# Performance work log

Measured on AMD Instinct MI355X. Metric: run time of the kernel, lower is better.

Reference implementation:

```python
import jax, jax.numpy as jnp
import numpy as np

SEQ = 4096
EMBED = 1024


def setup_inputs() -> dict:
    key = jax.random.key(0)
    k1, k2 = jax.random.split(key)
    x = jax.random.normal(k1, (SEQ, EMBED), dtype=jnp.float32)
    # torch Linear(embed, 3*embed): store transposed weight so y = x @ W + b
    W = jax.random.normal(k2, (EMBED, 3 * EMBED), dtype=jnp.float32) * (1.0 / np.sqrt(EMBED))
    b = jnp.zeros((3 * EMBED,), dtype=jnp.float32)
    return {"x": x, "W": W, "b": b}


def reference(x, W, b):
    # QKV projection: [S, 3E] -> chunk along features
    qkv = x @ W + b
    q, k, v = jnp.split(qkv, 3, axis=1)  # each [S, E]
    d = q.shape[-1]
    scale = jnp.sqrt(jnp.asarray(d, dtype=x.dtype))
    logits = (q @ k.T) / scale  # [S, S]
    S = q.shape[0]
    causal = jnp.triu(jnp.ones((S, S), dtype=bool), k=1)
    logits = jnp.where(causal, -jnp.inf, logits)
    w = jax.nn.softmax(logits, axis=1)
    return w @ v  # [S, E]
```

## Files before the change

kernel.cpp:

```cpp
#include <hip/hip_runtime.h>

typedef short s16x8 __attribute__((ext_vector_type(8)));
typedef unsigned short u16;
typedef u16 u16x8 __attribute__((ext_vector_type(8)));
typedef float f32x4 __attribute__((ext_vector_type(4)));

#define SEQ 4096
#define EMBED 1024
#define NQKV 3072

static __device__ __forceinline__ u16 f2bf(float f) {
  unsigned int u = __float_as_uint(f);
  u += 0x7fffu + ((u >> 16) & 1u);
  return (u16)(u >> 16);
}
static __device__ __forceinline__ float bf2f(u16 b) {
  return __uint_as_float(((unsigned int)b) << 16);
}

static __device__ __forceinline__ f32x4 mfma16(s16x8 a, s16x8 b, f32x4 c) {
  return __builtin_amdgcn_mfma_f32_16x16x32_bf16(a, b, c, 0, 0, 0);
}

static __device__ __forceinline__ void gl2lds(const u16* g, u16* l) {
  __builtin_amdgcn_global_load_lds(
      (const __attribute__((address_space(1))) unsigned int*)g,
      (__attribute__((address_space(3))) unsigned int*)l, 16, 0, 0);
}

#define WAITVM(n) asm volatile("s_waitcnt vmcnt(" #n ")" ::: "memory")
#define LGKM0 asm volatile("s_waitcnt lgkmcnt(0)" ::: "memory")
#define BAR() asm volatile("s_waitcnt lgkmcnt(0)\n\ts_barrier" ::: "memory")

__global__ __launch_bounds__(256) void conv_x(const float* __restrict__ x,
                                              u16* __restrict__ xbf) {
  const size_t base = ((size_t)blockIdx.x * 256 + threadIdx.x) * 16;
  u16 tmp[16];
#pragma unroll
  for (int p = 0; p < 4; ++p) {
    float4 v = *reinterpret_cast<const float4*>(&x[base + p * 4]);
    tmp[p * 4 + 0] = f2bf(v.x); tmp[p * 4 + 1] = f2bf(v.y);
    tmp[p * 4 + 2] = f2bf(v.z); tmp[p * 4 + 3] = f2bf(v.w);
  }
  *reinterpret_cast<u16x8*>(&xbf[base]) = *reinterpret_cast<u16x8*>(&tmp[0]);
  *reinterpret_cast<u16x8*>(&xbf[base + 8]) = *reinterpret_cast<u16x8*>(&tmp[8]);
}

__global__ __launch_bounds__(256) void conv_wT(const float* __restrict__ W,
                                               u16* __restrict__ wT) {
  __shared__ u16 t[64][72];
  const int n0 = blockIdx.x * 64;
  const int k0 = blockIdx.y * 64;
  const int tid = threadIdx.x;
  const int rr = tid >> 3, c8 = (tid & 7) * 8;
#pragma unroll
  for (int p = 0; p < 2; ++p) {
    int r = p * 32 + rr;
    float4 a = *reinterpret_cast<const float4*>(&W[(size_t)(k0 + r) * NQKV + n0 + c8]);
    float4 b = *reinterpret_cast<const float4*>(&W[(size_t)(k0 + r) * NQKV + n0 + c8 + 4]);
    t[r][c8 + 0] = f2bf(a.x); t[r][c8 + 1] = f2bf(a.y);
    t[r][c8 + 2] = f2bf(a.z); t[r][c8 + 3] = f2bf(a.w);
    t[r][c8 + 4] = f2bf(b.x); t[r][c8 + 5] = f2bf(b.y);
    t[r][c8 + 6] = f2bf(b.z); t[r][c8 + 7] = f2bf(b.w);
  }
  __syncthreads();
#pragma unroll
  for (int p = 0; p < 2; ++p) {
    int c = p * 32 + rr;
    u16x8 v;
#pragma unroll
    for (int j = 0; j < 8; ++j) v[j] = t[c8 + j][c];
    *reinterpret_cast<u16x8*>(&wT[(size_t)(n0 + c) * EMBED + k0 + c8]) = v;
  }
}

#define GSTAGE32(dst, srcbase, stride)                                        \
  {                                                                           \
    _Pragma("unroll") for (int p_ = 0; p_ < 2; ++p_) {                        \
      gl2lds((srcbase) + (size_t)(p_ * 64 + w * 16 + (l >> 2)) * (stride) +   \
                 (l & 3) * 8,                                                 \
             (dst) + p_ * 2048 + w * 512);                                    \
    }                                                                         \
  }

#define MFMA_STEP(Acur, Bcur)                                                 \
  {                                                                           \
    s16x8 af[4], bfr[4];                                                      \
    _Pragma("unroll") for (int mb = 0; mb < 4; ++mb)                          \
        af[mb] = *reinterpret_cast<const s16x8*>(&(Acur)[(wr + mb * 16 + lr) * 32 + lg * 8]); \
    _Pragma("unroll") for (int nb = 0; nb < 4; ++nb)                          \
        bfr[nb] = *reinterpret_cast<const s16x8*>(&(Bcur)[(wc + nb * 16 + lr) * 32 + lg * 8]); \
    _Pragma("unroll") for (int mb = 0; mb < 4; ++mb)                          \
        _Pragma("unroll") for (int nb = 0; nb < 4; ++nb)                      \
            acc[mb][nb] = mfma16(af[mb], bfr[nb], acc[mb][nb]);               \
  }

#define KLOOP(n, SRC_A, SA_STRIDE, SRC_B, SB_STRIDE)                          \
  GSTAGE32(As[0], SRC_A(0), SA_STRIDE);                                       \
  GSTAGE32(Bs[0], SRC_B(0), SB_STRIDE);                                       \
  GSTAGE32(As[1], SRC_A(1), SA_STRIDE);                                       \
  GSTAGE32(Bs[1], SRC_B(1), SB_STRIDE);                                       \
  for (int t = 0; t < (n); ++t) {                                             \
    const int cur = t % 3;                                                    \
    if (t + 2 < (n)) {                                                        \
      LGKM0;                                                                  \
      const int nx = (t + 2) % 3;                                             \
      GSTAGE32(As[nx], SRC_A(t + 2), SA_STRIDE);                              \
      GSTAGE32(Bs[nx], SRC_B(t + 2), SB_STRIDE);                              \
      WAITVM(8);                                                              \
    } else if (t + 1 < (n)) {                                                 \
      WAITVM(4);                                                              \
    } else {                                                                  \
      WAITVM(0);                                                              \
    }                                                                         \
    BAR();                                                                    \
    MFMA_STEP(As[cur], Bs[cur]);                                              \
    BAR();                                                                    \
  }

__global__ __launch_bounds__(256) void qkv_gemm(const u16* __restrict__ xbf,
                                                const u16* __restrict__ wT,
                                                const float* __restrict__ bias,
                                                u16* __restrict__ qkv) {
  __shared__ u16 As[3][4096];
  __shared__ u16 Bs[3][4096];
  const int b = blockIdx.x;
  const int bs = (b & 7) * 96 + (b >> 3);
  const int bm = bs / 24, bn = bs % 24;
  const int m0 = bm * 128, n0 = bn * 128;
  const int tid = threadIdx.x;
  const int w = tid >> 6, l = tid & 63;
  const int wr = (w >> 1) * 64, wc = (w & 1) * 64;
  const int lg = l >> 4, lr = l & 15;

  f32x4 acc[4][4];
#pragma unroll
  for (int i = 0; i < 4; ++i)
#pragma unroll
    for (int j = 0; j < 4; ++j) acc[i][j] = (f32x4){0.f, 0.f, 0.f, 0.f};

  const u16* xa = xbf + (size_t)m0 * EMBED;
  const u16* wb = wT + (size_t)n0 * EMBED;
#define QA_SRC(t) (xa + (t) * 32)
#define QB_SRC(t) (wb + (t) * 32)
  KLOOP(32, QA_SRC, EMBED, QB_SRC, EMBED);
#undef QA_SRC
#undef QB_SRC

#pragma unroll
  for (int mb = 0; mb < 4; ++mb)
#pragma unroll
    for (int nb = 0; nb < 4; ++nb) {
      const int col = n0 + wc + nb * 16 + lr;
      const float bv = bias[col];
#pragma unroll
      for (int e = 0; e < 4; ++e) {
        const int row = m0 + wr + mb * 16 + lg * 4 + e;
        qkv[(size_t)row * NQKV + col] = f2bf(acc[mb][nb][e] + bv);
      }
    }
}

__global__ __launch_bounds__(256) void v_transpose(const u16* __restrict__ qkv,
                                                   u16* __restrict__ vT) {
  __shared__ u16 t[64][72];
  const int s0 = blockIdx.x * 64;
  const int c0 = blockIdx.y * 64;
  const int tid = threadIdx.x;
  const int rr = tid >> 3, c8 = (tid & 7) * 8;
#pragma unroll
  for (int p = 0; p < 2; ++p) {
    int r = p * 32 + rr;
    *reinterpret_cast<u16x8*>(&t[r][c8]) =
        *reinterpret_cast<const u16x8*>(&qkv[(size_t)(s0 + r) * NQKV + 2 * EMBED + c0 + c8]);
  }
  __syncthreads();
#pragma unroll
  for (int p = 0; p < 2; ++p) {
    int c = p * 32 + rr;
    u16x8 v;
#pragma unroll
    for (int j = 0; j < 8; ++j) v[j] = t[c8 + j][c];
    *reinterpret_cast<u16x8*>(&vT[(size_t)(c0 + c) * SEQ + s0 + c8]) = v;
  }
}

__global__ __launch_bounds__(256) void s_gemm(const u16* __restrict__ qkv,
                                              u16* __restrict__ Sp) {
  __shared__ u16 As[3][4096];
  __shared__ u16 Bs[3][4096];
  const int b = blockIdx.x;
  const int bs = (b & 7) * 66 + (b >> 3);
  int mt = 0, cum = 0;
  while (cum + mt + 1 <= bs) { cum += mt + 1; ++mt; }
  const int nt = bs - cum;
  const int m0 = mt * 128, n0 = nt * 128;
  const int tid = threadIdx.x;
  const int w = tid >> 6, l = tid & 63;
  const int wr = (w >> 1) * 64, wc = (w & 1) * 64;
  const int lg = l >> 4, lr = l & 15;

  f32x4 acc[4][4];
#pragma unroll
  for (int i = 0; i < 4; ++i)
#pragma unroll
    for (int j = 0; j < 4; ++j) acc[i][j] = (f32x4){0.f, 0.f, 0.f, 0.f};

  const u16* qa = qkv + (size_t)m0 * NQKV;
  const u16* kb = qkv + (size_t)n0 * NQKV + EMBED;
#define SA_SRC(t) (qa + (t) * 32)
#define SB_SRC(t) (kb + (t) * 32)
  KLOOP(32, SA_SRC, NQKV, SB_SRC, NQKV);
#undef SA_SRC
#undef SB_SRC

  u16* base = Sp + (size_t)bs * 16384;
#pragma unroll
  for (int mb = 0; mb < 4; ++mb)
#pragma unroll
    for (int nb = 0; nb < 4; ++nb) {
      const int cn = wc + nb * 16 + lr;
#pragma unroll
      for (int e = 0; e < 4; ++e) {
        const int rm = wr + mb * 16 + lg * 4 + e;
        base[rm * 128 + cn] = f2bf(acc[mb][nb][e] * 0.03125f);
      }
    }
}

__global__ __launch_bounds__(256) void softmax_rows(u16* __restrict__ Sp) {
  __shared__ float red[8];
  const int bid = blockIdx.x;
  const int tid = threadIdx.x;
  const int w = tid >> 6, l = tid & 63;
  const float NEG = -3.0e38f;

  for (int half = 0; half < 2; ++half) {
    const int r = half ? (4095 - bid) : bid;
    const int mt = r >> 7, rr = r & 127;
    const int Lp = (mt + 1) << 7;
    const size_t tri = (size_t)mt * (mt + 1) / 2;

    float v[16];
    float mx = NEG;
#pragma unroll
    for (int s = 0; s < 2; ++s) {
      const int j = tid * 8 + s * 2048;
      if (j < Lp) {
        const u16* p = Sp + (tri + (j >> 7)) * 16384 + rr * 128 + (j & 127);
        u16x8 xv = *reinterpret_cast<const u16x8*>(p);
#pragma unroll
        for (int e = 0; e < 8; ++e) {
          float f = (j + e <= r) ? bf2f(xv[e]) : NEG;
          v[s * 8 + e] = f;
          mx = fmaxf(mx, f);
        }
      } else {
#pragma unroll
        for (int e = 0; e < 8; ++e) v[s * 8 + e] = NEG;
      }
    }
#pragma unroll
    for (int off = 32; off >= 1; off >>= 1) mx = fmaxf(mx, __shfl_xor(mx, off, 64));
    if (l == 0) red[w] = mx;
    __syncthreads();
    mx = fmaxf(fmaxf(red[0], red[1]), fmaxf(red[2], red[3]));

    float sum = 0.f;
#pragma unroll
    for (int i = 0; i < 16; ++i) {
      float e = __expf(v[i] - mx);
      v[i] = e;
      sum += e;
    }
#pragma unroll
    for (int off = 32; off >= 1; off >>= 1) sum += __shfl_xor(sum, off, 64);
    if (l == 0) red[4 + w] = sum;
    __syncthreads();
    sum = red[4] + red[5] + red[6] + red[7];
    const float inv = 1.f / sum;

#pragma unroll
    for (int s = 0; s < 2; ++s) {
      const int j = tid * 8 + s * 2048;
      if (j < Lp) {
        u16x8 pk;
#pragma unroll
        for (int e = 0; e < 8; ++e) pk[e] = f2bf(v[s * 8 + e] * inv);
        *reinterpret_cast<u16x8*>(Sp + (tri + (j >> 7)) * 16384 + rr * 128 + (j & 127)) = pk;
      }
    }
    __syncthreads();
  }
}

__global__ __launch_bounds__(256) void pv_gemm(const u16* __restrict__ Sp,
                                               const u16* __restrict__ vT,
                                               float* __restrict__ out) {
  __shared__ u16 As[3][4096];
  __shared__ u16 Bs[3][4096];
  const int nt = blockIdx.y;
  int sx = blockIdx.x;
  int mt = 0, cum = 0, ls = 0;
  for (;;) {
    const int ns = (mt + 4) >> 2;
    if (sx < cum + ns) { ls = sx - cum; break; }
    cum += ns; ++mt;
  }
  const int m0 = mt * 128, n0 = nt * 128;
  const int k0 = ls * 512;
  const int kext = (mt + 1) * 128;
  const int kend = (k0 + 512 < kext) ? (k0 + 512) : kext;
  const int ksteps = (kend - k0) >> 5;
  const size_t tri = (size_t)mt * (mt + 1) / 2;

  const int tid = threadIdx.x;
  const int w = tid >> 6, l = tid & 63;
  const int wr = (w >> 1) * 64, wc = (w & 1) * 64;
  const int lg = l >> 4, lr = l & 15;

  f32x4 acc[4][4];
#pragma unroll
  for (int i = 0; i < 4; ++i)
#pragma unroll
    for (int j = 0; j < 4; ++j) acc[i][j] = (f32x4){0.f, 0.f, 0.f, 0.f};

#define PA_SRC(t) (Sp + (tri + ((k0 + (t)*32) >> 7)) * 16384 + ((k0 + (t)*32) & 127))
#define PB_SRC(t) (vT + (size_t)n0 * SEQ + k0 + (t)*32)
  KLOOP(ksteps, PA_SRC, 128, PB_SRC, SEQ);
#undef PA_SRC
#undef PB_SRC

#pragma unroll
  for (int mb = 0; mb < 4; ++mb)
#pragma unroll
    for (int nb = 0; nb < 4; ++nb) {
      const int col = n0 + wc + nb * 16 + lr;
#pragma unroll
      for (int e = 0; e < 4; ++e) {
        const int row = m0 + wr + mb * 16 + lg * 4 + e;
        unsafeAtomicAdd(&out[(size_t)row * EMBED + col], acc[mb][nb][e]);
      }
    }
}

__global__ __launch_bounds__(512) void attn_fb(const u16* __restrict__ qkv,
                                               const u16* __restrict__ vT,
                                               float* __restrict__ out) {
  __shared__ u16 q_lds[16][1032];
  __shared__ u16 kv_lds[8][3][2048];
  __shared__ u16 p_lds[16][136];
  __shared__ float redmax[8][16];
  __shared__ float redsum[8][16];
  const int bid = blockIdx.x;
  const int tid = threadIdx.x;
  const int w = tid >> 6, l = tid & 63;
  const int lg = l >> 4, lr = l & 15;

  const int sr = l >> 4;
  const int scb = (l & 15) * 16;
  const int scolA = ((scb ^ (sr << 4)) >> 1);
  const int scolB = ((scb ^ ((4 + sr) << 4)) >> 1);
  int boff[4];
#pragma unroll
  for (int kk = 0; kk < 4; ++kk)
    boff[kk] = lr * 256 + ((kk * 64 + lg * 16) ^ ((lr & 7) << 4));

  u16* kvb[3] = {&kv_lds[w][0][0], &kv_lds[w][1][0], &kv_lds[w][2][0]};

#define STAGE_K(dc, bufp)                                                     \
  {                                                                           \
    LGKM0;                                                                    \
    const u16* g0 = qkv + (size_t)(kb + w * 16 + sr) * NQKV + EMBED + (dc) * 128; \
    gl2lds(g0 + scolA, (bufp));                                               \
    gl2lds(g0 + 4 * NQKV + scolB, (bufp) + 512);                              \
    gl2lds(g0 + 8 * NQKV + scolA, (bufp) + 1024);                             \
    gl2lds(g0 + 12 * NQKV + scolB, (bufp) + 1536);                            \
  }
#define STAGE_V(j, bufp)                                                      \
  {                                                                           \
    LGKM0;                                                                    \
    const u16* g0 = vT + (size_t)((j) * 128 + w * 16 + sr) * SEQ + kb;        \
    gl2lds(g0 + scolA, (bufp));                                               \
    gl2lds(g0 + 4 * SEQ + scolB, (bufp) + 512);                               \
    gl2lds(g0 + 8 * SEQ + scolA, (bufp) + 1024);                              \
    gl2lds(g0 + 12 * SEQ + scolB, (bufp) + 1536);                             \
  }

  const int qb = bid * 16;
  __syncthreads();
#pragma unroll
  for (int p = 0; p < 4; ++p) {
    int idx = p * 512 + tid;
    int r = idx >> 7, c = (idx & 127) * 8;
    *reinterpret_cast<u16x8*>(&q_lds[r][c]) =
        *reinterpret_cast<const u16x8*>(&qkv[(size_t)(qb + r) * NQKV + c]);
  }
  __syncthreads();
  s16x8 qf[32];
#pragma unroll
  for (int kk = 0; kk < 32; ++kk)
    qf[kk] = *reinterpret_cast<const s16x8*>(&q_lds[lr][kk * 32 + lg * 8]);

  f32x4 o_acc[8];
#pragma unroll
  for (int j = 0; j < 8; ++j) o_acc[j] = (f32x4){0.f, 0.f, 0.f, 0.f};
  float m_st[4], l_st[4];
#pragma unroll
  for (int e = 0; e < 4; ++e) { m_st[e] = -__builtin_inff(); l_st[e] = 0.f; }

  const int n_it = (qb >> 7) + 1;
  for (int it = 0; it < n_it; ++it) {
    const int kb = it << 7;
    const int kcol = kb + w * 16 + lr;

    f32x4 s = (f32x4){0.f, 0.f, 0.f, 0.f};
    STAGE_K(0, kvb[0]);
    STAGE_K(1, kvb[1]);
#pragma unroll
    for (int dc = 0; dc < 8; ++dc) {
      if (dc < 6) {
        STAGE_K(dc + 2, kvb[(dc + 2) % 3]);
      } else if (dc == 6) {
        STAGE_V(0, kvb[2]);
      } else {
        STAGE_V(1, kvb[0]);
      }
      WAITVM(8);
      u16* cur = kvb[dc % 3];
#pragma unroll
      for (int kk = 0; kk < 4; ++kk) {
        s16x8 bfr = *reinterpret_cast<const s16x8*>((const char*)cur + boff[kk]);
        s = mfma16(qf[dc * 4 + kk], bfr, s);
      }
    }

    float sv[4], mx[4];
#pragma unroll
    for (int e = 0; e < 4; ++e) {
      float v = s[e] * 0.03125f;
      sv[e] = (kcol > qb + lg * 4 + e) ? -__builtin_inff() : v;
      mx[e] = sv[e];
    }
#pragma unroll
    for (int off = 1; off < 16; off <<= 1)
#pragma unroll
      for (int e = 0; e < 4; ++e) mx[e] = fmaxf(mx[e], __shfl_xor(mx[e], off, 64));
    if (lr == 0) {
#pragma unroll
      for (int e = 0; e < 4; ++e) redmax[w][lg * 4 + e] = mx[e];
    }
    BAR();

    float m_new[4], sc[4], pv[4], rs[4];
#pragma unroll
    for (int e = 0; e < 4; ++e) {
      float m = m_st[e];
#pragma unroll
      for (int ww = 0; ww < 8; ++ww) m = fmaxf(m, redmax[ww][lg * 4 + e]);
      m_new[e] = m;
      sc[e] = __expf(m_st[e] - m);
      pv[e] = __expf(sv[e] - m);
      rs[e] = pv[e];
    }
#pragma unroll
    for (int off = 1; off < 16; off <<= 1)
#pragma unroll
      for (int e = 0; e < 4; ++e) rs[e] += __shfl_xor(rs[e], off, 64);
    if (lr == 0) {
#pragma unroll
      for (int e = 0; e < 4; ++e) redsum[w][lg * 4 + e] = rs[e];
    }
#pragma unroll
    for (int e = 0; e < 4; ++e) p_lds[lg * 4 + e][w * 16 + lr] = f2bf(pv[e]);
    BAR();

#pragma unroll
    for (int e = 0; e < 4; ++e) {
      float a2 = l_st[e] * sc[e];
#pragma unroll
      for (int ww = 0; ww < 8; ++ww) a2 += redsum[ww][lg * 4 + e];
      l_st[e] = a2;
      m_st[e] = m_new[e];
    }
#pragma unroll
    for (int j = 0; j < 8; ++j)
#pragma unroll
      for (int e = 0; e < 4; ++e) o_acc[j][e] *= sc[e];

    s16x8 pa[4];
#pragma unroll
    for (int kk = 0; kk < 4; ++kk)
      pa[kk] = *reinterpret_cast<const s16x8*>(&p_lds[lr][kk * 32 + lg * 8]);

#pragma unroll
    for (int j = 0; j < 8; ++j) {
      if (j < 6) {
        STAGE_V(j + 2, kvb[(j + 4) % 3]);
        WAITVM(8);
      } else if (j == 6) {
        WAITVM(4);
      } else {
        WAITVM(0);
      }
      u16* cur = kvb[(j + 2) % 3];
#pragma unroll
      for (int kk = 0; kk < 4; ++kk) {
        s16x8 bfr = *reinterpret_cast<const s16x8*>((const char*)cur + boff[kk]);
        o_acc[j] = mfma16(pa[kk], bfr, o_acc[j]);
      }
    }
  }

#pragma unroll
  for (int j = 0; j < 8; ++j) {
    const int col = j * 128 + w * 16 + lr;
#pragma unroll
    for (int e = 0; e < 4; ++e)
      out[(size_t)(qb + lg * 4 + e) * EMBED + col] = o_acc[j][e] / l_st[e];
  }
#undef STAGE_K
#undef STAGE_V
}

extern "C" void kernel_launch(void* const* d_in, const int* in_sizes, int n_in,
                              void* d_out, int out_size, void* d_ws, size_t ws_size,
                              hipStream_t stream) {
  (void)in_sizes; (void)n_in; (void)out_size;
  const float* x = (const float*)d_in[0];
  const float* W = (const float*)d_in[1];
  const float* bias = (const float*)d_in[2];
  float* out = (float*)d_out;

  u16* qkv = (u16*)d_ws;
  u16* vT = qkv + (size_t)SEQ * NQKV;
  u16* xbf = vT;
  u16* wT = (u16*)d_out;
  u16* Sp = (u16*)((char*)d_ws + (32u << 20));

  const size_t need = (32u << 20) + (size_t)528 * 16384 * 2;

  conv_x<<<(SEQ * EMBED) / (256 * 16), 256, 0, stream>>>(x, xbf);
  conv_wT<<<dim3(NQKV / 64, EMBED / 64), 256, 0, stream>>>(W, wT);
  qkv_gemm<<<(SEQ / 128) * (NQKV / 128), 256, 0, stream>>>(xbf, wT, bias, qkv);
  v_transpose<<<dim3(SEQ / 64, EMBED / 64), 256, 0, stream>>>(qkv, vT);

  if (ws_size >= need) {
    s_gemm<<<528, 256, 0, stream>>>(qkv, Sp);
    softmax_rows<<<2048, 256, 0, stream>>>(Sp);
    hipMemsetAsync(d_out, 0, (size_t)SEQ * EMBED * sizeof(float), stream);
    pv_gemm<<<dim3(144, 8), 256, 0, stream>>>(Sp, vT, out);
  } else {
    attn_fb<<<SEQ / 16, 512, 0, stream>>>(qkv, vT, out);
  }
}
```

Before: 180.4 us.

## Use 256x256 tiles with 8 waves and interleaved prefetch/MFMA phases in GEMMs

All three GEMMs (QKV, scores, PV) move from 128x128 tiles with 4 waves to 256x256 tiles with 8 waves. They now share a core loop that splits each k-step into four phases, each overlapping one global-to-LDS stage load with MFMA work, with barriers and s_setprio between phases. The larger tiles cut global/LDS traffic per flop and the phasing aims to hide load latency. The cost is far fewer blocks (192, 136 and 160), which can leave CUs idle on a large GPU and worsens load imbalance across causal triangle tiles.

Result: faster. 161.4 us (-10.5%).

```diff
diff --git a/kernel.cpp b/kernel.cpp
--- a/kernel.cpp
+++ b/kernel.cpp
@@ -30,7 +30,7 @@
 
 #define WAITVM(n) asm volatile("s_waitcnt vmcnt(" #n ")" ::: "memory")
 #define LGKM0 asm volatile("s_waitcnt lgkmcnt(0)" ::: "memory")
-#define BAR() asm volatile("s_waitcnt lgkmcnt(0)\n\ts_barrier" ::: "memory")
+#define BARRIER() __builtin_amdgcn_s_barrier()
 
 __global__ __launch_bounds__(256) void conv_x(const float* __restrict__ x,
                                               u16* __restrict__ xbf) {
@@ -74,89 +74,94 @@
   }
 }
 
-#define GSTAGE32(dst, srcbase, stride)                                        \
+
+#define G256_PHASE(p, stgsrc, stgdst_off)                                     \
   {                                                                           \
-    _Pragma("unroll") for (int p_ = 0; p_ < 2; ++p_) {                        \
-      gl2lds((srcbase) + (size_t)(p_ * 64 + w * 16 + (l >> 2)) * (stride) +   \
-                 (l & 3) * 8,                                                 \
-             (dst) + p_ * 2048 + w * 512);                                    \
+    s16x8 a0_ = *reinterpret_cast<const s16x8*>(                              \
+        &lds_[aoff_ + (wm * 128 + (2 * (p)) * 16 + lr) * 32 + lg * 8]);       \
+    s16x8 a1_ = *reinterpret_cast<const s16x8*>(                              \
+        &lds_[aoff_ + (wm * 128 + (2 * (p) + 1) * 16 + lr) * 32 + lg * 8]);   \
+    if (stg_) gl2lds((stgsrc), lds_ + (stgdst_off) + w * 512);                \
+    BARRIER();                                                                \
+    LGKM0;                                                                    \
+    __builtin_amdgcn_s_setprio(1);                                            \
+    _Pragma("unroll") for (int ni = 0; ni < 4; ++ni) {                        \
+      acc[2 * (p)][ni] = mfma16(a0_, bf_[ni], acc[2 * (p)][ni]);              \
+      acc[2 * (p) + 1][ni] = mfma16(a1_, bf_[ni], acc[2 * (p) + 1][ni]);      \
     }                                                                         \
-  }
-
-#define MFMA_STEP(Acur, Bcur)                                                 \
-  {                                                                           \
-    s16x8 af[4], bfr[4];                                                      \
-    _Pragma("unroll") for (int mb = 0; mb < 4; ++mb)                          \
-        af[mb] = *reinterpret_cast<const s16x8*>(&(Acur)[(wr + mb * 16 + lr) * 32 + lg * 8]); \
-    _Pragma("unroll") for (int nb = 0; nb < 4; ++nb)                          \
-        bfr[nb] = *reinterpret_cast<const s16x8*>(&(Bcur)[(wc + nb * 16 + lr) * 32 + lg * 8]); \
-    _Pragma("unroll") for (int mb = 0; mb < 4; ++mb)                          \
-        _Pragma("unroll") for (int nb = 0; nb < 4; ++nb)                      \
-            acc[mb][nb] = mfma16(af[mb], bfr[nb], acc[mb][nb]);               \
-  }
-
-#define KLOOP(n, SRC_A, SA_STRIDE, SRC_B, SB_STRIDE)                          \
-  GSTAGE32(As[0], SRC_A(0), SA_STRIDE);                                       \
-  GSTAGE32(Bs[0], SRC_B(0), SB_STRIDE);                                       \
-  GSTAGE32(As[1], SRC_A(1), SA_STRIDE);                                       \
-  GSTAGE32(Bs[1], SRC_B(1), SB_STRIDE);                                       \
-  for (int t = 0; t < (n); ++t) {                                             \
-    const int cur = t % 3;                                                    \
-    if (t + 2 < (n)) {                                                        \
-      LGKM0;                                                                  \
-      const int nx = (t + 2) % 3;                                             \
-      GSTAGE32(As[nx], SRC_A(t + 2), SA_STRIDE);                              \
-      GSTAGE32(Bs[nx], SRC_B(t + 2), SB_STRIDE);                              \
-      WAITVM(8);                                                              \
-    } else if (t + 1 < (n)) {                                                 \
-      WAITVM(4);                                                              \
-    } else {                                                                  \
-      WAITVM(0);                                                              \
-    }                                                                         \
-    BAR();                                                                    \
-    MFMA_STEP(As[cur], Bs[cur]);                                              \
-    BAR();                                                                    \
-  }
-
-__global__ __launch_bounds__(256) void qkv_gemm(const u16* __restrict__ xbf,
+    __builtin_amdgcn_s_setprio(0);                                            \
+  }
+
+#define G256_CORE(NSTEPS, SRCA, SRCB)                                         \
+  f32x4 acc[8][4];                                                            \
+  _Pragma("unroll") for (int i_ = 0; i_ < 8; ++i_)                            \
+  _Pragma("unroll") for (int j_ = 0; j_ < 4; ++j_)                            \
+      acc[i_][j_] = (f32x4){0.f, 0.f, 0.f, 0.f};                              \
+  gl2lds(SRCA(0, 0), lds_ + w * 512);                                         \
+  gl2lds(SRCA(0, 1), lds_ + 4096 + w * 512);                                  \
+  gl2lds(SRCB(0, 0), lds_ + 24576 + w * 512);                                 \
+  gl2lds(SRCB(0, 1), lds_ + 24576 + 4096 + w * 512);                          \
+  gl2lds(SRCA(1, 0), lds_ + 8192 + w * 512);                                  \
+  gl2lds(SRCA(1, 1), lds_ + 8192 + 4096 + w * 512);                           \
+  gl2lds(SRCB(1, 0), lds_ + 24576 + 8192 + w * 512);                          \
+  gl2lds(SRCB(1, 1), lds_ + 24576 + 8192 + 4096 + w * 512);                   \
+  WAITVM(4);                                                                  \
+  BARRIER();                                                                  \
+  int cb_ = 0;                                                                \
+  for (int kt = 0; kt < (NSTEPS); ++kt) {                                     \
+    int nb_ = cb_ + 2; if (nb_ >= 3) nb_ -= 3;                                \
+    const int aoff_ = cb_ * 8192;                                             \
+    const int boff_ = 24576 + cb_ * 8192;                                     \
+    const int an_ = nb_ * 8192;                                               \
+    const int bn_ = 24576 + nb_ * 8192;                                       \
+    const bool stg_ = (kt + 2) < (NSTEPS);                                    \
+    s16x8 bf_[4];                                                             \
+    _Pragma("unroll") for (int ni = 0; ni < 4; ++ni)                          \
+        bf_[ni] = *reinterpret_cast<const s16x8*>(                            \
+            &lds_[boff_ + (wn * 64 + ni * 16 + lr) * 32 + lg * 8]);           \
+    G256_PHASE(0, SRCA(kt + 2, 0), an_)                                       \
+    BARRIER();                                                                \
+    G256_PHASE(1, SRCA(kt + 2, 1), an_ + 4096)                                \
+    BARRIER();                                                                \
+    G256_PHASE(2, SRCB(kt + 2, 0), bn_)                                       \
+    BARRIER();                                                                \
+    G256_PHASE(3, SRCB(kt + 2, 1), bn_ + 4096)                                \
+    if (stg_) { WAITVM(4); } else { WAITVM(0); }                              \
+    BARRIER();                                                                \
+    cb_ = (cb_ + 1 == 3) ? 0 : cb_ + 1;                                       \
+  }
+
+__global__ __launch_bounds__(512) void qkv_gemm(const u16* __restrict__ xbf,
                                                 const u16* __restrict__ wT,
                                                 const float* __restrict__ bias,
                                                 u16* __restrict__ qkv) {
-  __shared__ u16 As[3][4096];
-  __shared__ u16 Bs[3][4096];
+  __shared__ u16 lds_[49152];
   const int b = blockIdx.x;
-  const int bs = (b & 7) * 96 + (b >> 3);
-  const int bm = bs / 24, bn = bs % 24;
-  const int m0 = bm * 128, n0 = bn * 128;
+  const int bs = (b & 7) * 24 + (b >> 3);
+  const int m0 = (bs / 12) * 256, n0 = (bs % 12) * 256;
   const int tid = threadIdx.x;
   const int w = tid >> 6, l = tid & 63;
-  const int wr = (w >> 1) * 64, wc = (w & 1) * 64;
+  const int wm = w >> 2, wn = w & 3;
   const int lg = l >> 4, lr = l & 15;
 
-  f32x4 acc[4][4];
-#pragma unroll
-  for (int i = 0; i < 4; ++i)
-#pragma unroll
-    for (int j = 0; j < 4; ++j) acc[i][j] = (f32x4){0.f, 0.f, 0.f, 0.f};
-
-  const u16* xa = xbf + (size_t)m0 * EMBED;
-  const u16* wb = wT + (size_t)n0 * EMBED;
-#define QA_SRC(t) (xa + (t) * 32)
-#define QB_SRC(t) (wb + (t) * 32)
-  KLOOP(32, QA_SRC, EMBED, QB_SRC, EMBED);
-#undef QA_SRC
-#undef QB_SRC
-
-#pragma unroll
-  for (int mb = 0; mb < 4; ++mb)
-#pragma unroll
-    for (int nb = 0; nb < 4; ++nb) {
-      const int col = n0 + wc + nb * 16 + lr;
+  const u16* Ab = xbf + (size_t)m0 * EMBED;
+  const u16* Bb = wT + (size_t)n0 * EMBED;
+#define QSRCA(kt, i) (Ab + (size_t)(((i)*8 + w) * 16 + (l >> 2)) * EMBED + (kt)*32 + (l & 3) * 8)
+#define QSRCB(kt, i) (Bb + (size_t)(((i)*8 + w) * 16 + (l >> 2)) * EMBED + (kt)*32 + (l & 3) * 8)
+  G256_CORE(32, QSRCA, QSRCB)
+#undef QSRCA
+#undef QSRCB
+
+#pragma unroll
+  for (int mi = 0; mi < 8; ++mi)
+#pragma unroll
+    for (int ni = 0; ni < 4; ++ni) {
+      const int col = n0 + wn * 64 + ni * 16 + lr;
       const float bv = bias[col];
 #pragma unroll
       for (int e = 0; e < 4; ++e) {
-        const int row = m0 + wr + mb * 16 + lg * 4 + e;
-        qkv[(size_t)row * NQKV + col] = f2bf(acc[mb][nb][e] + bv);
+        const int row = m0 + wm * 128 + mi * 16 + lg * 4 + e;
+        qkv[(size_t)row * NQKV + col] = f2bf(acc[mi][ni][e] + bv);
       }
     }
 }
@@ -185,45 +190,38 @@
   }
 }
 
-__global__ __launch_bounds__(256) void s_gemm(const u16* __restrict__ qkv,
+__global__ __launch_bounds__(512) void s_gemm(const u16* __restrict__ qkv,
                                               u16* __restrict__ Sp) {
-  __shared__ u16 As[3][4096];
-  __shared__ u16 Bs[3][4096];
+  __shared__ u16 lds_[49152];
   const int b = blockIdx.x;
-  const int bs = (b & 7) * 66 + (b >> 3);
+  const int bs = (b & 7) * 17 + (b >> 3);
   int mt = 0, cum = 0;
   while (cum + mt + 1 <= bs) { cum += mt + 1; ++mt; }
   const int nt = bs - cum;
-  const int m0 = mt * 128, n0 = nt * 128;
+  const int m0 = mt * 256, n0 = nt * 256;
   const int tid = threadIdx.x;
   const int w = tid >> 6, l = tid & 63;
-  const int wr = (w >> 1) * 64, wc = (w & 1) * 64;
+  const int wm = w >> 2, wn = w & 3;
   const int lg = l >> 4, lr = l & 15;
 
-  f32x4 acc[4][4];
-#pragma unroll
-  for (int i = 0; i < 4; ++i)
-#pragma unroll
-    for (int j = 0; j < 4; ++j) acc[i][j] = (f32x4){0.f, 0.f, 0.f, 0.f};
-
-  const u16* qa = qkv + (size_t)m0 * NQKV;
-  const u16* kb = qkv + (size_t)n0 * NQKV + EMBED;
-#define SA_SRC(t) (qa + (t) * 32)
-#define SB_SRC(t) (kb + (t) * 32)
-  KLOOP(32, SA_SRC, NQKV, SB_SRC, NQKV);
-#undef SA_SRC
-#undef SB_SRC
-
-  u16* base = Sp + (size_t)bs * 16384;
-#pragma unroll
-  for (int mb = 0; mb < 4; ++mb)
-#pragma unroll
-    for (int nb = 0; nb < 4; ++nb) {
-      const int cn = wc + nb * 16 + lr;
+  const u16* Ab = qkv + (size_t)m0 * NQKV;
+  const u16* Bb = qkv + (size_t)n0 * NQKV + EMBED;
+#define SSRCA(kt, i) (Ab + (size_t)(((i)*8 + w) * 16 + (l >> 2)) * NQKV + (kt)*32 + (l & 3) * 8)
+#define SSRCB(kt, i) (Bb + (size_t)(((i)*8 + w) * 16 + (l >> 2)) * NQKV + (kt)*32 + (l & 3) * 8)
+  G256_CORE(32, SSRCA, SSRCB)
+#undef SSRCA
+#undef SSRCB
+
+  u16* base = Sp + (size_t)bs * 65536;
+#pragma unroll
+  for (int mi = 0; mi < 8; ++mi)
+#pragma unroll
+    for (int ni = 0; ni < 4; ++ni) {
+      const int cn = wn * 64 + ni * 16 + lr;
 #pragma unroll
       for (int e = 0; e < 4; ++e) {
-        const int rm = wr + mb * 16 + lg * 4 + e;
-        base[rm * 128 + cn] = f2bf(acc[mb][nb][e] * 0.03125f);
+        const int rm = wm * 128 + mi * 16 + lg * 4 + e;
+        base[rm * 256 + cn] = f2bf(acc[mi][ni][e] * 0.03125f);
       }
     }
 }
@@ -237,8 +235,8 @@
 
   for (int half = 0; half < 2; ++half) {
     const int r = half ? (4095 - bid) : bid;
-    const int mt = r >> 7, rr = r & 127;
-    const int Lp = (mt + 1) << 7;
+    const int mt = r >> 8, rr = r & 255;
+    const int Lp = (mt + 1) << 8;
     const size_t tri = (size_t)mt * (mt + 1) / 2;
 
     float v[16];
@@ -247,7 +245,7 @@
     for (int s = 0; s < 2; ++s) {
       const int j = tid * 8 + s * 2048;
       if (j < Lp) {
-        const u16* p = Sp + (tri + (j >> 7)) * 16384 + rr * 128 + (j & 127);
+        const u16* p = Sp + (tri + (j >> 8)) * 65536 + rr * 256 + (j & 255);
         u16x8 xv = *reinterpret_cast<const u16x8*>(p);
 #pragma unroll
         for (int e = 0; e < 8; ++e) {
@@ -287,59 +285,60 @@
         u16x8 pk;
 #pragma unroll
         for (int e = 0; e < 8; ++e) pk[e] = f2bf(v[s * 8 + e] * inv);
-        *reinterpret_cast<u16x8*>(Sp + (tri + (j >> 7)) * 16384 + rr * 128 + (j & 127)) = pk;
+        *reinterpret_cast<u16x8*>(Sp + (tri + (j >> 8)) * 65536 + rr * 256 + (j & 255)) = pk;
       }
     }
     __syncthreads();
   }
 }
 
-__global__ __launch_bounds__(256) void pv_gemm(const u16* __restrict__ Sp,
+__global__ __launch_bounds__(512) void pv_gemm(const u16* __restrict__ Sp,
                                                const u16* __restrict__ vT,
                                                float* __restrict__ out) {
-  __shared__ u16 As[3][4096];
-  __shared__ u16 Bs[3][4096];
-  const int nt = blockIdx.y;
-  int sx = blockIdx.x;
-  int mt = 0, cum = 0, ls = 0;
+  __shared__ u16 lds_[49152];
+  const int b = blockIdx.x;
+  const int bs = (b & 7) * 20 + (b >> 3);
+  int sx = bs, mt = 0, cum = 0;
   for (;;) {
-    const int ns = (mt + 4) >> 2;
-    if (sx < cum + ns) { ls = sx - cum; break; }
-    cum += ns; ++mt;
-  }
-  const int m0 = mt * 128, n0 = nt * 128;
-  const int k0 = ls * 512;
-  const int kext = (mt + 1) * 128;
-  const int kend = (k0 + 512 < kext) ? (k0 + 512) : kext;
+    const int cnt = ((mt + 4) >> 2) * 4;
+    if (sx < cum + cnt) break;
+    cum += cnt; ++mt;
+  }
+  const int rem = sx - cum;
+  const int ns = (mt + 4) >> 2;
+  const int nt = rem / ns, ls = rem % ns;
+  const int m0 = mt * 256, n0 = nt * 256;
+  const int k0 = ls * 1024;
+  const int kext = (mt + 1) << 8;
+  const int kend = (k0 + 1024 < kext) ? (k0 + 1024) : kext;
   const int ksteps = (kend - k0) >> 5;
   const size_t tri = (size_t)mt * (mt + 1) / 2;
 
   const int tid = threadIdx.x;
   const int w = tid >> 6, l = tid & 63;
-  const int wr = (w >> 1) * 64, wc = (w & 1) * 64;
+  const int wm = w >> 2, wn = w & 3;
   const int lg = l >> 4, lr = l & 15;
 
-  f32x4 acc[4][4];
-#pragma unroll
-  for (int i = 0; i < 4; ++i)
-#pragma unroll
-    for (int j = 0; j < 4; ++j) acc[i][j] = (f32x4){0.f, 0.f, 0.f, 0.f};
-
-#define PA_SRC(t) (Sp + (tri + ((k0 + (t)*32) >> 7)) * 16384 + ((k0 + (t)*32) & 127))
-#define PB_SRC(t) (vT + (size_t)n0 * SEQ + k0 + (t)*32)
-  KLOOP(ksteps, PA_SRC, 128, PB_SRC, SEQ);
-#undef PA_SRC
-#undef PB_SRC
-
-#pragma unroll
-  for (int mb = 0; mb < 4; ++mb)
-#pragma unroll
-    for (int nb = 0; nb < 4; ++nb) {
-      const int col = n0 + wc + nb * 16 + lr;
+#define PSRCA(kt, i)                                                          \
+  (Sp + (tri + ((unsigned)(k0 + (kt)*32) >> 8)) * 65536 +                     \
+   (size_t)(((i)*8 + w) * 16 + (l >> 2)) * 256 + ((k0 + (kt)*32) & 255) +     \
+   (l & 3) * 8)
+#define PSRCB(kt, i)                                                          \
+  (vT + (size_t)(n0 + ((i)*8 + w) * 16 + (l >> 2)) * SEQ + k0 + (kt)*32 +     \
+   (l & 3) * 8)
+  G256_CORE(ksteps, PSRCA, PSRCB)
+#undef PSRCA
+#undef PSRCB
+
+#pragma unroll
+  for (int mi = 0; mi < 8; ++mi)
+#pragma unroll
+    for (int ni = 0; ni < 4; ++ni) {
+      const int col = n0 + wn * 64 + ni * 16 + lr;
 #pragma unroll
       for (int e = 0; e < 4; ++e) {
-        const int row = m0 + wr + mb * 16 + lg * 4 + e;
-        unsafeAtomicAdd(&out[(size_t)row * EMBED + col], acc[mb][nb][e]);
+        const int row = m0 + wm * 128 + mi * 16 + lg * 4 + e;
+        unsafeAtomicAdd(&out[(size_t)row * EMBED + col], acc[mi][ni][e]);
       }
     }
 }
@@ -450,7 +449,7 @@
 #pragma unroll
       for (int e = 0; e < 4; ++e) redmax[w][lg * 4 + e] = mx[e];
     }
-    BAR();
+    asm volatile("s_waitcnt lgkmcnt(0)\n\ts_barrier" ::: "memory");
 
     float m_new[4], sc[4], pv[4], rs[4];
 #pragma unroll
@@ -473,7 +472,7 @@
     }
 #pragma unroll
     for (int e = 0; e < 4; ++e) p_lds[lg * 4 + e][w * 16 + lr] = f2bf(pv[e]);
-    BAR();
+    asm volatile("s_waitcnt lgkmcnt(0)\n\ts_barrier" ::: "memory");
 
 #pragma unroll
     for (int e = 0; e < 4; ++e) {
@@ -538,18 +537,18 @@
   u16* wT = (u16*)d_out;
   u16* Sp = (u16*)((char*)d_ws + (32u << 20));
 
-  const size_t need = (32u << 20) + (size_t)528 * 16384 * 2;
+  const size_t need = (32u << 20) + (size_t)136 * 65536 * 2;
 
   conv_x<<<(SEQ * EMBED) / (256 * 16), 256, 0, stream>>>(x, xbf);
   conv_wT<<<dim3(NQKV / 64, EMBED / 64), 256, 0, stream>>>(W, wT);
-  qkv_gemm<<<(SEQ / 128) * (NQKV / 128), 256, 0, stream>>>(xbf, wT, bias, qkv);
+  qkv_gemm<<<192, 512, 0, stream>>>(xbf, wT, bias, qkv);
   v_transpose<<<dim3(SEQ / 64, EMBED / 64), 256, 0, stream>>>(qkv, vT);
 
   if (ws_size >= need) {
-    s_gemm<<<528, 256, 0, stream>>>(qkv, Sp);
+    s_gemm<<<136, 512, 0, stream>>>(qkv, Sp);
     softmax_rows<<<2048, 256, 0, stream>>>(Sp);
     hipMemsetAsync(d_out, 0, (size_t)SEQ * EMBED * sizeof(float), stream);
-    pv_gemm<<<dim3(144, 8), 256, 0, stream>>>(Sp, vT, out);
+    pv_gemm<<<160, 512, 0, stream>>>(Sp, vT, out);
   } else {
     attn_fb<<<SEQ / 16, 512, 0, stream>>>(qkv, vT, out);
   }
```

## Fuse V transpose into QKV GEMM epilogue and switch to double-buffered LDS

Applied to the files above, without the earlier changes.

The V transpose kernel is removed. QKV GEMM blocks covering the V columns now stage their bf16 tile in LDS and write it out transposed directly into vT, which saves one kernel launch and a full read and write of V. The GEMM k-loop goes from triple to double buffering, so LDS per block shrinks and occupancy may rise, at the cost of less prefetch depth. pv_gemm split-K chunks double from 512 to 1024, giving fewer blocks and fewer atomic adds but less parallelism.

Measured after the change: 150.1 us (median of 2 runs). -16.8%, faster.

```diff
diff --git a/kernel.cpp b/kernel.cpp
--- a/kernel.cpp
+++ b/kernel.cpp
@@ -74,56 +74,54 @@
   }
 }
 
-#define GSTAGE32(dst, srcbase, stride)                                        \
+
+#define GSTAGE32(dst_off, srcbase, stride)                                    \
   {                                                                           \
     _Pragma("unroll") for (int p_ = 0; p_ < 2; ++p_) {                        \
       gl2lds((srcbase) + (size_t)(p_ * 64 + w * 16 + (l >> 2)) * (stride) +   \
                  (l & 3) * 8,                                                 \
-             (dst) + p_ * 2048 + w * 512);                                    \
+             lds_ + (dst_off) + p_ * 2048 + w * 512);                         \
     }                                                                         \
   }
 
-#define MFMA_STEP(Acur, Bcur)                                                 \
+#define MFMA_STEP(aoff, boff)                                                 \
   {                                                                           \
     s16x8 af[4], bfr[4];                                                      \
     _Pragma("unroll") for (int mb = 0; mb < 4; ++mb)                          \
-        af[mb] = *reinterpret_cast<const s16x8*>(&(Acur)[(wr + mb * 16 + lr) * 32 + lg * 8]); \
+        af[mb] = *reinterpret_cast<const s16x8*>(                             \
+            &lds_[(aoff) + (wr + mb * 16 + lr) * 32 + lg * 8]);               \
     _Pragma("unroll") for (int nb = 0; nb < 4; ++nb)                          \
-        bfr[nb] = *reinterpret_cast<const s16x8*>(&(Bcur)[(wc + nb * 16 + lr) * 32 + lg * 8]); \
+        bfr[nb] = *reinterpret_cast<const s16x8*>(                            \
+            &lds_[(boff) + (wc + nb * 16 + lr) * 32 + lg * 8]);               \
     _Pragma("unroll") for (int mb = 0; mb < 4; ++mb)                          \
         _Pragma("unroll") for (int nb = 0; nb < 4; ++nb)                      \
             acc[mb][nb] = mfma16(af[mb], bfr[nb], acc[mb][nb]);               \
   }
 
-#define KLOOP(n, SRC_A, SA_STRIDE, SRC_B, SB_STRIDE)                          \
-  GSTAGE32(As[0], SRC_A(0), SA_STRIDE);                                       \
-  GSTAGE32(Bs[0], SRC_B(0), SB_STRIDE);                                       \
-  GSTAGE32(As[1], SRC_A(1), SA_STRIDE);                                       \
-  GSTAGE32(Bs[1], SRC_B(1), SB_STRIDE);                                       \
+#define KLOOP2(n, SRC_A, SA_STRIDE, SRC_B, SB_STRIDE)                         \
+  GSTAGE32(0, SRC_A(0), SA_STRIDE);                                           \
+  GSTAGE32(8192, SRC_B(0), SB_STRIDE);                                        \
   for (int t = 0; t < (n); ++t) {                                             \
-    const int cur = t % 3;                                                    \
-    if (t + 2 < (n)) {                                                        \
+    const int cur_ = t & 1, nx_ = cur_ ^ 1;                                   \
+    if (t + 1 < (n)) {                                                        \
       LGKM0;                                                                  \
-      const int nx = (t + 2) % 3;                                             \
-      GSTAGE32(As[nx], SRC_A(t + 2), SA_STRIDE);                              \
-      GSTAGE32(Bs[nx], SRC_B(t + 2), SB_STRIDE);                              \
-      WAITVM(8);                                                              \
-    } else if (t + 1 < (n)) {                                                 \
+      GSTAGE32(nx_ * 4096, SRC_A(t + 1), SA_STRIDE);                          \
+      GSTAGE32(8192 + nx_ * 4096, SRC_B(t + 1), SB_STRIDE);                   \
       WAITVM(4);                                                              \
     } else {                                                                  \
       WAITVM(0);                                                              \
     }                                                                         \
     BAR();                                                                    \
-    MFMA_STEP(As[cur], Bs[cur]);                                              \
+    MFMA_STEP(cur_ * 4096, 8192 + cur_ * 4096);                               \
     BAR();                                                                    \
   }
 
 __global__ __launch_bounds__(256) void qkv_gemm(const u16* __restrict__ xbf,
                                                 const u16* __restrict__ wT,
                                                 const float* __restrict__ bias,
-                                                u16* __restrict__ qkv) {
-  __shared__ u16 As[3][4096];
-  __shared__ u16 Bs[3][4096];
+                                                u16* __restrict__ qkv,
+                                                u16* __restrict__ vT) {
+  __shared__ u16 lds_[17408];
   const int b = blockIdx.x;
   const int bs = (b & 7) * 96 + (b >> 3);
   const int bm = bs / 24, bn = bs % 24;
@@ -143,52 +141,51 @@
   const u16* wb = wT + (size_t)n0 * EMBED;
 #define QA_SRC(t) (xa + (t) * 32)
 #define QB_SRC(t) (wb + (t) * 32)
-  KLOOP(32, QA_SRC, EMBED, QB_SRC, EMBED);
+  KLOOP2(32, QA_SRC, EMBED, QB_SRC, EMBED);
 #undef QA_SRC
 #undef QB_SRC
 
-#pragma unroll
-  for (int mb = 0; mb < 4; ++mb)
-#pragma unroll
-    for (int nb = 0; nb < 4; ++nb) {
-      const int col = n0 + wc + nb * 16 + lr;
-      const float bv = bias[col];
-#pragma unroll
-      for (int e = 0; e < 4; ++e) {
-        const int row = m0 + wr + mb * 16 + lg * 4 + e;
-        qkv[(size_t)row * NQKV + col] = f2bf(acc[mb][nb][e] + bv);
-      }
-    }
-}
-
-__global__ __launch_bounds__(256) void v_transpose(const u16* __restrict__ qkv,
-                                                   u16* __restrict__ vT) {
-  __shared__ u16 t[64][72];
-  const int s0 = blockIdx.x * 64;
-  const int c0 = blockIdx.y * 64;
-  const int tid = threadIdx.x;
-  const int rr = tid >> 3, c8 = (tid & 7) * 8;
-#pragma unroll
-  for (int p = 0; p < 2; ++p) {
-    int r = p * 32 + rr;
-    *reinterpret_cast<u16x8*>(&t[r][c8]) =
-        *reinterpret_cast<const u16x8*>(&qkv[(size_t)(s0 + r) * NQKV + 2 * EMBED + c0 + c8]);
-  }
-  __syncthreads();
-#pragma unroll
-  for (int p = 0; p < 2; ++p) {
-    int c = p * 32 + rr;
-    u16x8 v;
-#pragma unroll
-    for (int j = 0; j < 8; ++j) v[j] = t[c8 + j][c];
-    *reinterpret_cast<u16x8*>(&vT[(size_t)(c0 + c) * SEQ + s0 + c8]) = v;
+  if (n0 < 2 * EMBED) {
+#pragma unroll
+    for (int mb = 0; mb < 4; ++mb)
+#pragma unroll
+      for (int nb = 0; nb < 4; ++nb) {
+        const int col = n0 + wc + nb * 16 + lr;
+        const float bv = bias[col];
+#pragma unroll
+        for (int e = 0; e < 4; ++e) {
+          const int row = m0 + wr + mb * 16 + lg * 4 + e;
+          qkv[(size_t)row * NQKV + col] = f2bf(acc[mb][nb][e] + bv);
+        }
+      }
+  } else {
+    const int vb = n0 - 2 * EMBED;
+    __syncthreads();
+#pragma unroll
+    for (int mb = 0; mb < 4; ++mb)
+#pragma unroll
+      for (int nb = 0; nb < 4; ++nb) {
+        const int cc = wc + nb * 16 + lr;
+        const float bv = bias[n0 + cc];
+#pragma unroll
+        for (int e = 0; e < 4; ++e)
+          lds_[(wr + mb * 16 + lg * 4 + e) * 136 + cc] = f2bf(acc[mb][nb][e] + bv);
+      }
+    __syncthreads();
+    const int c = tid >> 1, hf = tid & 1;
+#pragma unroll
+    for (int j = 0; j < 8; ++j) {
+      u16x8 v;
+#pragma unroll
+      for (int e2 = 0; e2 < 8; ++e2) v[e2] = lds_[(hf * 64 + j * 8 + e2) * 136 + c];
+      *reinterpret_cast<u16x8*>(&vT[(size_t)(vb + c) * SEQ + m0 + hf * 64 + j * 8]) = v;
+    }
   }
 }
 
 __global__ __launch_bounds__(256) void s_gemm(const u16* __restrict__ qkv,
                                               u16* __restrict__ Sp) {
-  __shared__ u16 As[3][4096];
-  __shared__ u16 Bs[3][4096];
+  __shared__ u16 lds_[16384];
   const int b = blockIdx.x;
   const int bs = (b & 7) * 66 + (b >> 3);
   int mt = 0, cum = 0;
@@ -210,7 +207,7 @@
   const u16* kb = qkv + (size_t)n0 * NQKV + EMBED;
 #define SA_SRC(t) (qa + (t) * 32)
 #define SB_SRC(t) (kb + (t) * 32)
-  KLOOP(32, SA_SRC, NQKV, SB_SRC, NQKV);
+  KLOOP2(32, SA_SRC, NQKV, SB_SRC, NQKV);
 #undef SA_SRC
 #undef SB_SRC
 
@@ -297,20 +294,19 @@
 __global__ __launch_bounds__(256) void pv_gemm(const u16* __restrict__ Sp,
                                                const u16* __restrict__ vT,
                                                float* __restrict__ out) {
-  __shared__ u16 As[3][4096];
-  __shared__ u16 Bs[3][4096];
+  __shared__ u16 lds_[16384];
   const int nt = blockIdx.y;
-  int sx = blockIdx.x;
+  int s81 = blockIdx.x;
   int mt = 0, cum = 0, ls = 0;
   for (;;) {
-    const int ns = (mt + 4) >> 2;
-    if (sx < cum + ns) { ls = sx - cum; break; }
+    const int ns = (mt + 8) >> 3;
+    if (s81 < cum + ns) { ls = s81 - cum; break; }
     cum += ns; ++mt;
   }
   const int m0 = mt * 128, n0 = nt * 128;
-  const int k0 = ls * 512;
+  const int k0 = ls * 1024;
   const int kext = (mt + 1) * 128;
-  const int kend = (k0 + 512 < kext) ? (k0 + 512) : kext;
+  const int kend = (k0 + 1024 < kext) ? (k0 + 1024) : kext;
   const int ksteps = (kend - k0) >> 5;
   const size_t tri = (size_t)mt * (mt + 1) / 2;
 
@@ -327,7 +323,7 @@
 
 #define PA_SRC(t) (Sp + (tri + ((k0 + (t)*32) >> 7)) * 16384 + ((k0 + (t)*32) & 127))
 #define PB_SRC(t) (vT + (size_t)n0 * SEQ + k0 + (t)*32)
-  KLOOP(ksteps, PA_SRC, 128, PB_SRC, SEQ);
+  KLOOP2(ksteps, PA_SRC, 128, PB_SRC, SEQ);
 #undef PA_SRC
 #undef PB_SRC
 
@@ -534,22 +530,22 @@
 
   u16* qkv = (u16*)d_ws;
   u16* vT = qkv + (size_t)SEQ * NQKV;
-  u16* xbf = vT;
   u16* wT = (u16*)d_out;
   u16* Sp = (u16*)((char*)d_ws + (32u << 20));
 
   const size_t need = (32u << 20) + (size_t)528 * 16384 * 2;
+  const bool big = ws_size >= need;
+  u16* xbf = big ? Sp : (u16*)((char*)d_out + (8u << 20));
 
   conv_x<<<(SEQ * EMBED) / (256 * 16), 256, 0, stream>>>(x, xbf);
   conv_wT<<<dim3(NQKV / 64, EMBED / 64), 256, 0, stream>>>(W, wT);
-  qkv_gemm<<<(SEQ / 128) * (NQKV / 128), 256, 0, stream>>>(xbf, wT, bias, qkv);
-  v_transpose<<<dim3(SEQ / 64, EMBED / 64), 256, 0, stream>>>(qkv, vT);
-
-  if (ws_size >= need) {
+  qkv_gemm<<<(SEQ / 128) * (NQKV / 128), 256, 0, stream>>>(xbf, wT, bias, qkv, vT);
+
+  if (big) {
     s_gemm<<<528, 256, 0, stream>>>(qkv, Sp);
     softmax_rows<<<2048, 256, 0, stream>>>(Sp);
     hipMemsetAsync(d_out, 0, (size_t)SEQ * EMBED * sizeof(float), stream);
-    pv_gemm<<<dim3(144, 8), 256, 0, stream>>>(Sp, vT, out);
+    pv_gemm<<<dim3(80, 8), 256, 0, stream>>>(Sp, vT, out);
   } else {
     attn_fb<<<SEQ / 16, 512, 0, stream>>>(qkv, vT, out);
   }
```
